# Kernel optimization log

Hardware: AMD Instinct MI355X
Metric: run time of the kernel (lower is better)

Reference implementation:

```python
import jax, jax.numpy as jnp
import numpy as np

B, P, L, M, L_EVAL = 8, 16, 256, 16, 2048
T_MAX = 100.0


def setup_inputs() -> dict:
    key = jax.random.key(0)
    k1, k2, k3, k4, k5 = jax.random.split(key, 5)
    # sorted event times per path (Hawkes event streams are ordered)
    event_times = jnp.sort(jax.random.uniform(k1, (B, P, L), dtype=jnp.float32) * T_MAX, axis=-1)
    # parameters are assumed already positive (post-softplus) -> uniform [0,1)
    mu = jax.random.uniform(k2, (B, M, P, L), dtype=jnp.float32)
    alpha = jax.random.uniform(k3, (B, M, P, L), dtype=jnp.float32)
    beta = jax.random.uniform(k4, (B, M, P, L), dtype=jnp.float32)
    query_times = jax.random.uniform(k5, (B, P, L_EVAL), dtype=jnp.float32) * T_MAX
    return {"query_times": query_times, "event_times": event_times,
            "mu": mu, "alpha": alpha, "beta": beta}


def reference(query_times, event_times, mu, alpha, beta):
    # query_times: [B,P,Le]; event_times: [B,P,L]; mu/alpha/beta: [B,M,P,L]
    b, m, p, l = mu.shape
    le = query_times.shape[-1]
    # index of latest event strictly before each query time (mask + max, as original)
    past_mask = event_times[:, :, None, :] < query_times[:, :, :, None]  # [B,P,Le,L]
    idx = jnp.arange(l, dtype=jnp.int32)
    last_idx = jnp.max(jnp.where(past_mask, idx, -1), axis=-1)            # [B,P,Le]
    ci = jnp.clip(last_idx, 0, None)
    gi = jnp.broadcast_to(ci[:, None, :, :], (b, m, p, le))
    mu_last = jnp.take_along_axis(mu, gi, axis=3)
    alpha_last = jnp.take_along_axis(alpha, gi, axis=3)
    beta_last = jnp.take_along_axis(beta, gi, axis=3)
    t_last = jnp.take_along_axis(event_times, ci, axis=2)                 # [B,P,Le]
    t_last = jnp.where(last_idx == -1, jnp.zeros_like(t_last), t_last)
    delta_t = (query_times - t_last)[:, None, :, :]                       # [B,1,P,Le]
    base = mu_last + (alpha_last - mu_last) * jnp.exp(-beta_last * delta_t)
    return jax.nn.softplus(base)                                          # [B,M,P,Le]
```

## Files before the change

### kernel.cpp

```cpp
#include <hip/hip_runtime.h>
#include <float.h>

#define BB  8
#define PP  16
#define LL  256
#define MM  16
#define LE  2048
#define NQ  (BB * PP * LE)

#define THREADS 256

__global__ __launch_bounds__(THREADS) void k_search(
    const float* __restrict__ qt,
    const float* __restrict__ ev,
    int*   __restrict__ ci_out,
    float* __restrict__ dt_out)
{
    __shared__ float ev_s[LL + 1];
    const int bp   = blockIdx.x >> 2;
    const int tile = blockIdx.x & 3;
    const int t = threadIdx.x;

    ev_s[t] = ev[bp * LL + t];
    if (t == 0) ev_s[LL] = FLT_MAX;
    __syncthreads();

    const int base = bp * LE + tile * 512;
    #pragma unroll
    for (int k = 0; k < 512; k += THREADS) {
        const int idx = base + k + t;
        const float q = qt[idx];
        int lo = 0, hi = LL;
        #pragma unroll
        for (int s = 0; s < 9; ++s) {
            const int mid = (lo + hi) >> 1;
            if (ev_s[mid] < q) lo = mid + 1; else hi = mid;
        }
        const int cnt = lo;
        const int ci  = (cnt > 0) ? (cnt - 1) : 0;
        const float t_last = (cnt > 0) ? ev_s[ci] : 0.0f;
        ci_out[idx] = ci;
        dt_out[idx] = q - t_last;
    }
}

#define MG   4
#define QT2  1024

__global__ __launch_bounds__(THREADS) void k_eval(
    const float* __restrict__ mu,
    const float* __restrict__ alpha,
    const float* __restrict__ beta,
    const int*   __restrict__ ci_in,
    const float* __restrict__ dt_in,
    float* __restrict__ out)
{
    __shared__ float4 pr[MG * LL];

    const int mg   =  blockIdx.x & 3;
    const int tile = (blockIdx.x >> 2) & 1;
    const int bp   =  blockIdx.x >> 3;
    const int b = bp / PP;
    const int p = bp % PP;
    const int t = threadIdx.x;

    {
        const float4* mu4 = (const float4*)mu;
        const float4* al4 = (const float4*)alpha;
        const float4* be4 = (const float4*)beta;
        const int i  = t;
        const int m  = i >> 6;
        const int l4 = i & 63;
        const int g  = ((b * MM + mg * MG + m) * PP + p) * (LL / 4) + l4;
        const float4 mv = mu4[g];
        const float4 av = al4[g];
        const float4 bv = be4[g];
        const int o = m * LL + l4 * 4;
        pr[o + 0] = make_float4(mv.x, av.x, bv.x, 0.0f);
        pr[o + 1] = make_float4(mv.y, av.y, bv.y, 0.0f);
        pr[o + 2] = make_float4(mv.z, av.z, bv.z, 0.0f);
        pr[o + 3] = make_float4(mv.w, av.w, bv.w, 0.0f);
    }
    __syncthreads();

    const int q0  = tile * QT2 + 4 * t;
    const int idx = bp * LE + q0;
    const int4   ci4 = *(const int4*)  (ci_in + idx);
    const float4 dt4 = *(const float4*)(dt_in + idx);
    const int ci[4] = {ci4.x, ci4.y, ci4.z, ci4.w};
    const float dt[4] = {dt4.x, dt4.y, dt4.z, dt4.w};

    #pragma unroll
    for (int m = 0; m < MG; ++m) {
        float r[4];
        #pragma unroll
        for (int j = 0; j < 4; ++j) {
            const float4 pm = pr[m * LL + ci[j]];
            const float e = __expf(-pm.z * dt[j]);
            const float v = pm.x + (pm.y - pm.x) * e;
            r[j] = __logf(1.0f + __expf(v));
        }
        float4* dst = (float4*)(out + ((size_t)(b * MM + mg * MG + m) * PP + p) * LE + q0);
        *dst = make_float4(r[0], r[1], r[2], r[3]);
    }
}

extern "C" void kernel_launch(void* const* d_in, const int* in_sizes, int n_in,
                              void* d_out, int out_size, void* d_ws, size_t ws_size,
                              hipStream_t stream) {
    const float* qt    = (const float*)d_in[0];
    const float* ev    = (const float*)d_in[1];
    const float* mu    = (const float*)d_in[2];
    const float* alpha = (const float*)d_in[3];
    const float* beta  = (const float*)d_in[4];
    float* out = (float*)d_out;

    int*   ci_ws = (int*)d_ws;
    float* dt_ws = (float*)((char*)d_ws + (size_t)NQ * sizeof(int));

    k_search<<<(BB * PP) * 4, THREADS, 0, stream>>>(qt, ev, ci_ws, dt_ws);
    k_eval<<<(BB * PP) * (MM / MG) * (LE / QT2), THREADS, 0, stream>>>(
        mu, alpha, beta, ci_ws, dt_ws, out);
}
```

Baseline: 79.29 us.

## Fuse event search into evaluation kernel, dropping workspace round-trip

Merges the binary-search kernel into the evaluation kernel. Each block now loads its path's event times into shared memory and searches its own queries, four interleaved searches per thread. This removes a launch and the global write and reread of the index and delta-time arrays. In exchange, each query is searched once per M-group block (four times in total), so the search work is recomputed.

Result: no change. 77.97 us (-1.7%).

```diff
diff --git a/kernel.cpp b/kernel.cpp
--- a/kernel.cpp
+++ b/kernel.cpp
@@ -6,55 +6,20 @@
 #define LL  256
 #define MM  16
 #define LE  2048
-#define NQ  (BB * PP * LE)
 
 #define THREADS 256
+#define MG   4
+#define QT   1024
 
-__global__ __launch_bounds__(THREADS) void k_search(
+__global__ __launch_bounds__(THREADS) void hawkes_fused(
     const float* __restrict__ qt,
     const float* __restrict__ ev,
-    int*   __restrict__ ci_out,
-    float* __restrict__ dt_out)
-{
-    __shared__ float ev_s[LL + 1];
-    const int bp   = blockIdx.x >> 2;
-    const int tile = blockIdx.x & 3;
-    const int t = threadIdx.x;
-
-    ev_s[t] = ev[bp * LL + t];
-    if (t == 0) ev_s[LL] = FLT_MAX;
-    __syncthreads();
-
-    const int base = bp * LE + tile * 512;
-    #pragma unroll
-    for (int k = 0; k < 512; k += THREADS) {
-        const int idx = base + k + t;
-        const float q = qt[idx];
-        int lo = 0, hi = LL;
-        #pragma unroll
-        for (int s = 0; s < 9; ++s) {
-            const int mid = (lo + hi) >> 1;
-            if (ev_s[mid] < q) lo = mid + 1; else hi = mid;
-        }
-        const int cnt = lo;
-        const int ci  = (cnt > 0) ? (cnt - 1) : 0;
-        const float t_last = (cnt > 0) ? ev_s[ci] : 0.0f;
-        ci_out[idx] = ci;
-        dt_out[idx] = q - t_last;
-    }
-}
-
-#define MG   4
-#define QT2  1024
-
-__global__ __launch_bounds__(THREADS) void k_eval(
     const float* __restrict__ mu,
     const float* __restrict__ alpha,
     const float* __restrict__ beta,
-    const int*   __restrict__ ci_in,
-    const float* __restrict__ dt_in,
     float* __restrict__ out)
 {
+    __shared__ float  ev_s[LL + 1];
     __shared__ float4 pr[MG * LL];
 
     const int mg   =  blockIdx.x & 3;
@@ -64,13 +29,15 @@
     const int p = bp % PP;
     const int t = threadIdx.x;
 
+    ev_s[t] = ev[bp * LL + t];
+    if (t == 0) ev_s[LL] = FLT_MAX;
+
     {
         const float4* mu4 = (const float4*)mu;
         const float4* al4 = (const float4*)alpha;
         const float4* be4 = (const float4*)beta;
-        const int i  = t;
-        const int m  = i >> 6;
-        const int l4 = i & 63;
+        const int m  = t >> 6;
+        const int l4 = t & 63;
         const int g  = ((b * MM + mg * MG + m) * PP + p) * (LL / 4) + l4;
         const float4 mv = mu4[g];
         const float4 av = al4[g];
@@ -83,12 +50,29 @@
     }
     __syncthreads();
 
-    const int q0  = tile * QT2 + 4 * t;
-    const int idx = bp * LE + q0;
-    const int4   ci4 = *(const int4*)  (ci_in + idx);
-    const float4 dt4 = *(const float4*)(dt_in + idx);
-    const int ci[4] = {ci4.x, ci4.y, ci4.z, ci4.w};
-    const float dt[4] = {dt4.x, dt4.y, dt4.z, dt4.w};
+    const int q0 = tile * QT + 4 * t;
+    const float4 qv = *(const float4*)(qt + bp * LE + q0);
+    const float q[4] = {qv.x, qv.y, qv.z, qv.w};
+
+    int lo[4] = {0, 0, 0, 0};
+    int hi[4] = {LL, LL, LL, LL};
+    #pragma unroll
+    for (int s = 0; s < 9; ++s) {
+        #pragma unroll
+        for (int j = 0; j < 4; ++j) {
+            const int mid = (lo[j] + hi[j]) >> 1;
+            if (ev_s[mid] < q[j]) lo[j] = mid + 1; else hi[j] = mid;
+        }
+    }
+    int   ci[4];
+    float dt[4];
+    #pragma unroll
+    for (int j = 0; j < 4; ++j) {
+        const int cnt = lo[j];
+        ci[j] = (cnt > 0) ? (cnt - 1) : 0;
+        const float t_last = (cnt > 0) ? ev_s[ci[j]] : 0.0f;
+        dt[j] = q[j] - t_last;
+    }
 
     #pragma unroll
     for (int m = 0; m < MG; ++m) {
@@ -115,10 +99,6 @@
     const float* beta  = (const float*)d_in[4];
     float* out = (float*)d_out;
 
-    int*   ci_ws = (int*)d_ws;
-    float* dt_ws = (float*)((char*)d_ws + (size_t)NQ * sizeof(int));
-
-    k_search<<<(BB * PP) * 4, THREADS, 0, stream>>>(qt, ev, ci_ws, dt_ws);
-    k_eval<<<(BB * PP) * (MM / MG) * (LE / QT2), THREADS, 0, stream>>>(
-        mu, alpha, beta, ci_ws, dt_ws, out);
+    const int nblocks = (BB * PP) * (LE / QT) * (MM / MG);
+    hawkes_fused<<<nblocks, THREADS, 0, stream>>>(qt, ev, mu, alpha, beta, out);
 }
```
